# Kernel tuning notes

Hardware: AMD Instinct MI355X
Metric: run time of the kernel (lower is better)

## Reference

```python
import jax, jax.numpy as jnp
import numpy as np

N = 100000   # nodes
E = 1600000  # edges
G = 512      # graphs
IN_F = 128
HID = 64
EPS = 1e-5


def setup_inputs() -> dict:
    key = jax.random.key(0)
    ks = jax.random.split(key, 16)
    x = jax.random.normal(ks[0], (N, IN_F), dtype=jnp.float32)
    edge_index = jax.random.randint(ks[1], (2, E), 0, N, dtype=jnp.int64)
    batch = jnp.sort(jax.random.randint(ks[2], (N,), 0, G, dtype=jnp.int64))
    s = 0.05
    return {
        'x': x, 'edge_index': edge_index, 'batch': batch,
        'W1': jax.random.normal(ks[3], (IN_F, HID), jnp.float32) * s,
        'b1': jax.random.normal(ks[4], (HID,), jnp.float32) * s,
        'g1': jax.random.uniform(ks[5], (HID,), jnp.float32),
        'be1': jax.random.normal(ks[6], (HID,), jnp.float32) * s,
        'rm1': jnp.zeros((HID,), jnp.float32),
        'rv1': jnp.ones((HID,), jnp.float32),
        'W2': jax.random.normal(ks[7], (HID, HID), jnp.float32) * s,
        'b2': jax.random.normal(ks[8], (HID,), jnp.float32) * s,
        'g2': jax.random.uniform(ks[9], (HID,), jnp.float32),
        'be2': jax.random.normal(ks[10], (HID,), jnp.float32) * s,
        'rm2': jnp.zeros((HID,), jnp.float32),
        'rv2': jnp.ones((HID,), jnp.float32),
        'Wh1': jax.random.normal(ks[11], (2 * HID, HID), jnp.float32) * s,
        'bh1': jax.random.normal(ks[12], (HID,), jnp.float32) * s,
        'Wh2': jax.random.normal(ks[13], (HID, HID // 2), jnp.float32) * s,
        'bh2': jnp.zeros((HID // 2,), jnp.float32),
        'Wh3': jax.random.normal(ks[14], (HID // 2, 1), jnp.float32) * s,
        'bh3': jnp.zeros((1,), jnp.float32),
    }


def _gcn(h, W, b, src, dst):
    # GCNConv with added self-loops and symmetric D^{-1/2} A D^{-1/2} normalization
    hw = h @ W                                   # [N, HID]
    deg = jnp.ones((N,), hw.dtype).at[dst].add(1.0)  # in-degree + self-loop
    dinv = jax.lax.rsqrt(deg)
    norm = dinv[src] * dinv[dst]                 # [E]
    agg = jax.ops.segment_sum(hw[src] * norm[:, None], dst, num_segments=N)
    return agg + hw * (dinv * dinv)[:, None] + b  # self-loop term + bias


def _bn(x, g, b, rm, rv):
    return (x - rm) * jax.lax.rsqrt(rv + EPS) * g + b


def reference(x, edge_index, batch, W1, b1, g1, be1, rm1, rv1,
              W2, b2, g2, be2, rm2, rv2, Wh1, bh1, Wh2, bh2, Wh3, bh3):
    src, dst = edge_index[0], edge_index[1]
    # layer 0 (no residual: dim change 128 -> 64)
    h = jax.nn.relu(_bn(_gcn(x, W1, b1, src, dst), g1, be1, rm1, rv1))
    # layer 1 with residual
    h = h + jax.nn.relu(_bn(_gcn(h, W2, b2, src, dst), g2, be2, rm2, rv2))
    # global mean + max pooling per graph
    ones = jnp.ones((N,), h.dtype)
    cnt = jnp.maximum(jax.ops.segment_sum(ones, batch, num_segments=G), 1.0)
    h_mean = jax.ops.segment_sum(h, batch, num_segments=G) / cnt[:, None]
    h_max = jax.ops.segment_max(h, batch, num_segments=G)
    hg = jnp.concatenate([h_mean, h_max], axis=-1)   # [G, 2*HID]
    # MLP head (dropout disabled in eval)
    z = jax.nn.relu(hg @ Wh1 + bh1)
    z = jax.nn.relu(z @ Wh2 + bh2)
    out = z @ Wh3 + bh3
    return jax.nn.sigmoid(out).squeeze(-1)           # [G]
```

## Files before the change

### kernel.cpp

```cpp
#include <hip/hip_runtime.h>
#include <math.h>

#define NN 100000
#define EE 1600000
#define GG 512
#define INF_ 128
#define HID 64
#define EPS 1e-5f

#define NBUK 391
#define P1_TILES 98
#define P1_PAD 104
#define GB_B 25
#define GEMM1_B 1563

typedef unsigned int uint32;
typedef __attribute__((ext_vector_type(8))) short bf16x8;
typedef __attribute__((ext_vector_type(4))) float f32x4;
typedef __attribute__((ext_vector_type(2))) float f32x2;

static __device__ inline uint32 f2bf(float f) {
    uint32 u = __float_as_uint(f);
    return (u + 0x7FFFu + ((u >> 16) & 1u)) >> 16;
}


template <int K, bool SCALE>
__device__ __forceinline__ void gemm_body(const float* __restrict__ X,
        const float* __restrict__ W, const float* __restrict__ dinv,
        uint32* __restrict__ outb, int nrows, int bx,
        unsigned short* __restrict__ Al, unsigned short* __restrict__ Bl) {
    constexpr int KP = K + 8;
    int tid = threadIdx.x;
    for (int i = tid; i < 64 * (K / 2); i += 256) {
        int n = i & 63, kp = i >> 6;
        uint32 lo = f2bf(W[(size_t)(2 * kp) * 64 + n]);
        uint32 hi = f2bf(W[(size_t)(2 * kp + 1) * 64 + n]);
        *(uint32*)&Bl[n * KP + kp * 2] = lo | (hi << 16);
    }
    int r0 = bx * 64;
    const float* Xb = X + (size_t)r0 * K;
    int limit = (nrows - r0) * K;
    for (int f = tid * 4; f < 64 * K; f += 1024) {
        float4 v = {0.f, 0.f, 0.f, 0.f};
        if (f + 3 < limit) v = *(const float4*)&Xb[f];
        int row = f / K, kpos = f % K;
        ushort4 pk;
        pk.x = (unsigned short)f2bf(v.x);
        pk.y = (unsigned short)f2bf(v.y);
        pk.z = (unsigned short)f2bf(v.z);
        pk.w = (unsigned short)f2bf(v.w);
        *(ushort4*)&Al[row * KP + kpos] = pk;
    }
    __syncthreads();
    int lane = tid & 63, wv = tid >> 6;
    int m = lane & 15, quad = lane >> 4;
    f32x4 acc0 = {0.f, 0.f, 0.f, 0.f}, acc1 = acc0, acc2 = acc0, acc3 = acc0;
    int arow = wv * 16 + m;
#pragma unroll
    for (int k0 = 0; k0 < K; k0 += 32) {
        int koff = k0 + quad * 8;
        bf16x8 a = *(const bf16x8*)&Al[arow * KP + koff];
        bf16x8 b0 = *(const bf16x8*)&Bl[(0 * 16 + m) * KP + koff];
        bf16x8 b1 = *(const bf16x8*)&Bl[(1 * 16 + m) * KP + koff];
        bf16x8 b2 = *(const bf16x8*)&Bl[(2 * 16 + m) * KP + koff];
        bf16x8 b3 = *(const bf16x8*)&Bl[(3 * 16 + m) * KP + koff];
        acc0 = __builtin_amdgcn_mfma_f32_16x16x32_bf16(a, b0, acc0, 0, 0, 0);
        acc1 = __builtin_amdgcn_mfma_f32_16x16x32_bf16(a, b1, acc1, 0, 0, 0);
        acc2 = __builtin_amdgcn_mfma_f32_16x16x32_bf16(a, b2, acc2, 0, 0, 0);
        acc3 = __builtin_amdgcn_mfma_f32_16x16x32_bf16(a, b3, acc3, 0, 0, 0);
    }
    float dv[4];
#pragma unroll
    for (int reg = 0; reg < 4; ++reg) {
        int row = r0 + wv * 16 + quad * 4 + reg;
        if (SCALE) dv[reg] = (row < nrows) ? dinv[row] : 0.f;
        else       dv[reg] = 1.f;
    }
    const float* accs[4] = {(const float*)&acc0, (const float*)&acc1,
                            (const float*)&acc2, (const float*)&acc3};
#pragma unroll
    for (int nt = 0; nt < 4; ++nt) {
#pragma unroll
        for (int reg = 0; reg < 4; ++reg) {
            float val = accs[nt][reg] * dv[reg];
            float v1 = __shfl_down(val, 1);
            float v2 = __shfl_down(val, 2);
            float v3 = __shfl_down(val, 3);
            int row = r0 + wv * 16 + quad * 4 + reg;
            if (((m & 3) == 0) && row < nrows) {
                int u = __builtin_amdgcn_cvt_pk_fp8_f32(val, v1, 0, false);
                u = __builtin_amdgcn_cvt_pk_fp8_f32(v2, v3, u, true);
                outb[(size_t)row * 16 + nt * 4 + (m >> 2)] = (uint32)u;
            }
        }
    }
}

__global__ __launch_bounds__(256) void k_mega(const int* __restrict__ ei,
        int* __restrict__ hblk, const int* __restrict__ bat, int* __restrict__ gb,
        const float* __restrict__ x, const float* __restrict__ W1,
        uint32* __restrict__ hwb,
        const float* b1, const float* g1, const float* be1,
        const float* rm1, const float* rv1,
        const float* b2, const float* g2, const float* be2,
        const float* rm2, const float* rv2, float* sc) {
    __shared__ alignas(16) char smem[64 * (INF_ + 8) * 2 * 2];
    int b = blockIdx.x, t = threadIdx.x;
    if (b < P1_TILES) {
        int* h = (int*)smem;
        for (int i = t; i < NBUK; i += 256) h[i] = 0;
        __syncthreads();
        const int4* dst4 = (const int4*)(ei + EE);
        int base4 = b * 4096;
        for (int j = 0; j < 16; ++j) {
            int i4 = base4 + j * 256 + t;
            if (i4 < EE / 4) {
                int4 d = dst4[i4];
                atomicAdd(&h[d.x >> 8], 1);
                atomicAdd(&h[d.y >> 8], 1);
                atomicAdd(&h[d.z >> 8], 1);
                atomicAdd(&h[d.w >> 8], 1);
            }
        }
        __syncthreads();
        for (int i = t; i < NBUK; i += 256) hblk[i * P1_PAD + b] = h[i];
    } else if (b < P1_TILES + GB_B) {
        int gid = (b - P1_TILES) * 256 + t;
        for (int i = gid; i < NN; i += GB_B * 256) {
            int bi = bat[i];
            if (i == 0) {
                for (int g = 0; g <= bi; ++g) gb[g] = 0;
            } else {
                int bp = bat[i - 1];
                for (int g = bp + 1; g <= bi; ++g) gb[g] = i;
            }
            if (i == NN - 1)
                for (int g = bi + 1; g <= GG; ++g) gb[g] = NN;
        }
    } else if (b < P1_TILES + GB_B + 1) {
        if (t < 64) {
            int l = t;
            float s1 = g1[l] * rsqrtf(rv1[l] + EPS);
            sc[l]       = s1;
            sc[64 + l]  = (b1[l] - rm1[l]) * s1 + be1[l];
            float s2 = g2[l] * rsqrtf(rv2[l] + EPS);
            sc[128 + l] = s2;
            sc[192 + l] = (b2[l] - rm2[l]) * s2 + be2[l];
        } else if (t < 80) {
            hwb[(size_t)NN * 16 + (t - 64)] = 0u;
        }
        for (int i = t; i < NBUK * (P1_PAD - P1_TILES); i += 256) {
            int k = i / (P1_PAD - P1_TILES);
            int bb = P1_TILES + i % (P1_PAD - P1_TILES);
            hblk[k * P1_PAD + bb] = 0;
        }
    } else {
        int bx = b - P1_TILES - GB_B - 1;
        unsigned short* Al = (unsigned short*)smem;
        unsigned short* Bl = (unsigned short*)(smem + 64 * (INF_ + 8) * 2);
        gemm_body<INF_, false>(x, W1, nullptr, hwb, NN, bx, Al, Bl);
    }
}

__global__ __launch_bounds__(512) void k_p1b(const int* __restrict__ ei,
                                             const int* __restrict__ hblk,
                                             uint32* __restrict__ pairs,
                                             int* __restrict__ bbase,
                                             int* __restrict__ offs) {
    __shared__ int h[NBUK];
    __shared__ int wsum[8];
    int b = blockIdx.x, t = threadIdx.x;
    int part = 0, c = 0;
    if (t < NBUK) {
        const int4* row = (const int4*)(hblk + t * P1_PAD);
#pragma unroll
        for (int q = 0; q < P1_PAD / 4; ++q) {
            int4 v = row[q];
            c += v.x + v.y + v.z + v.w;
            part += ((4 * q + 0 < b) ? v.x : 0) + ((4 * q + 1 < b) ? v.y : 0)
                  + ((4 * q + 2 < b) ? v.z : 0) + ((4 * q + 3 < b) ? v.w : 0);
        }
    }
    int lane = t & 63, w = t >> 6;
    int v = c;
    for (int d = 1; d < 64; d <<= 1) { int n = __shfl_up(v, d); if (lane >= d) v += n; }
    if (lane == 63) wsum[w] = v;
    __syncthreads();
    int pre = 0;
    for (int q = 0; q < w; ++q) pre += wsum[q];
    int excl = pre + v - c;
    if (t < NBUK) h[t] = excl + part;
    if (b == 0) {
        if (t <= NBUK) bbase[t] = excl;
        if (t == 0) offs[NN] = EE;
    }
    __syncthreads();
    const int4* src4 = (const int4*)ei;
    const int4* dst4 = (const int4*)(ei + EE);
    int base4 = b * 4096;
    for (int j = 0; j < 8; ++j) {
        int i4 = base4 + j * 512 + t;
        if (i4 < EE / 4) {
            int4 d = dst4[i4];
            int4 s = src4[i4];
            int p0 = atomicAdd(&h[d.x >> 8], 1);
            pairs[p0] = ((uint32)s.x << 8) | (uint32)(d.x & 255);
            int p1 = atomicAdd(&h[d.y >> 8], 1);
            pairs[p1] = ((uint32)s.y << 8) | (uint32)(d.y & 255);
            int p2 = atomicAdd(&h[d.z >> 8], 1);
            pairs[p2] = ((uint32)s.z << 8) | (uint32)(d.z & 255);
            int p3 = atomicAdd(&h[d.w >> 8], 1);
            pairs[p3] = ((uint32)s.w << 8) | (uint32)(d.w & 255);
        }
    }
}

__global__ __launch_bounds__(256) void k_p2(const uint32* __restrict__ pairs,
                                            const int* __restrict__ bbase,
                                            int* __restrict__ offs, float* __restrict__ dinv,
                                            int* __restrict__ col) {
    int b = blockIdx.x, t = threadIdx.x;
    int nbase = b << 8;
    int ebase = bbase[b], eend = bbase[b + 1];
    int m = eend - ebase;
    __shared__ int cnt[256];
    __shared__ int wsum[4];
    cnt[t] = 0;
    __syncthreads();
    for (int i = t; i < m; i += 256)
        atomicAdd(&cnt[pairs[ebase + i] & 255u], 1);
    __syncthreads();
    int c = cnt[t];
    int lane = t & 63, w = t >> 6;
    int v = c;
    for (int d = 1; d < 64; d <<= 1) { int n = __shfl_up(v, d); if (lane >= d) v += n; }
    if (lane == 63) wsum[w] = v;
    __syncthreads();
    int pre = 0;
    for (int q = 0; q < w; ++q) pre += wsum[q];
    int excl = pre + v - c;
    int node = nbase + t;
    if (node < NN) {
        offs[node] = ebase + excl;
        dinv[node] = rsqrtf(1.f + (float)c);
    }
    __syncthreads();
    cnt[t] = excl;
    __syncthreads();
    for (int i = t; i < m; i += 256) {
        uint32 u = pairs[ebase + i];
        int loc = atomicAdd(&cnt[u & 255u], 1);
        col[ebase + loc] = (int)(u >> 8);
    }
}

__global__ void k_gcn_gather_w(const uint32* __restrict__ hwb, const int* __restrict__ col,
                               const int* __restrict__ offs,
                               const float* __restrict__ dinv, const float* __restrict__ scale,
                               const float* __restrict__ shift,
                               float* __restrict__ out) {
    int node = blockIdx.x * 4 + (threadIdx.x >> 6);
    if (node >= NN) return;
    int lane = threadIdx.x & 63;
    int quarter = lane >> 4;
    int fl = lane & 15;
    int e0 = offs[node], e1 = offs[node + 1];
    float di = dinv[node];
    uint32 uself = hwb[(size_t)node * 16 + fl];
    float a0 = 0.f, a1 = 0.f, a2 = 0.f, a3 = 0.f;
    float b0 = 0.f, b1 = 0.f, b2 = 0.f, b3 = 0.f;
    for (int base = e0; base < e1; base += 64) {
        int m = e1 - base; if (m > 64) m = 64;
        int srcv = NN; float wv = 0.f;
        if (lane < m) { srcv = col[base + lane]; wv = dinv[srcv]; }
        for (int j = 0; j < m; j += 16) {
            int   s0 = __shfl(srcv, j + quarter);
            int   s1 = __shfl(srcv, j + 4 + quarter);
            int   s2 = __shfl(srcv, j + 8 + quarter);
            int   s3 = __shfl(srcv, j + 12 + quarter);
            float w0 = __shfl(wv, j + quarter);
            float w1 = __shfl(wv, j + 4 + quarter);
            float w2 = __shfl(wv, j + 8 + quarter);
            float w3 = __shfl(wv, j + 12 + quarter);
            uint32 u0 = hwb[(size_t)s0 * 16 + fl];
            uint32 u1 = hwb[(size_t)s1 * 16 + fl];
            uint32 u2 = hwb[(size_t)s2 * 16 + fl];
            uint32 u3 = hwb[(size_t)s3 * 16 + fl];
            f32x2 l0 = __builtin_amdgcn_cvt_pk_f32_fp8((int)u0, false);
            f32x2 h0 = __builtin_amdgcn_cvt_pk_f32_fp8((int)u0, true);
            f32x2 l1 = __builtin_amdgcn_cvt_pk_f32_fp8((int)u1, false);
            f32x2 h1 = __builtin_amdgcn_cvt_pk_f32_fp8((int)u1, true);
            f32x2 l2 = __builtin_amdgcn_cvt_pk_f32_fp8((int)u2, false);
            f32x2 h2 = __builtin_amdgcn_cvt_pk_f32_fp8((int)u2, true);
            f32x2 l3 = __builtin_amdgcn_cvt_pk_f32_fp8((int)u3, false);
            f32x2 h3 = __builtin_amdgcn_cvt_pk_f32_fp8((int)u3, true);
            a0 = fmaf(l0[0], w0, a0); a1 = fmaf(l0[1], w0, a1);
            a2 = fmaf(h0[0], w0, a2); a3 = fmaf(h0[1], w0, a3);
            b0 = fmaf(l1[0], w1, b0); b1 = fmaf(l1[1], w1, b1);
            b2 = fmaf(h1[0], w1, b2); b3 = fmaf(h1[1], w1, b3);
            a0 = fmaf(l2[0], w2, a0); a1 = fmaf(l2[1], w2, a1);
            a2 = fmaf(h2[0], w2, a2); a3 = fmaf(h2[1], w2, a3);
            b0 = fmaf(l3[0], w3, b0); b1 = fmaf(l3[1], w3, b1);
            b2 = fmaf(h3[0], w3, b2); b3 = fmaf(h3[1], w3, b3);
        }
    }
    a0 += b0; a1 += b1; a2 += b2; a3 += b3;
    a0 += __shfl_xor(a0, 16); a0 += __shfl_xor(a0, 32);
    a1 += __shfl_xor(a1, 16); a1 += __shfl_xor(a1, 32);
    a2 += __shfl_xor(a2, 16); a2 += __shfl_xor(a2, 32);
    a3 += __shfl_xor(a3, 16); a3 += __shfl_xor(a3, 32);
    if (quarter == 0) {
        f32x2 slo = __builtin_amdgcn_cvt_pk_f32_fp8((int)uself, false);
        f32x2 shi = __builtin_amdgcn_cvt_pk_f32_fp8((int)uself, true);
        float dii = di * di;
        float4 sc4 = *(const float4*)&scale[4 * fl];
        float4 sh4 = *(const float4*)&shift[4 * fl];
        float v0 = fmaf(a0 * di + slo[0] * dii, sc4.x, sh4.x);
        float v1 = fmaf(a1 * di + slo[1] * dii, sc4.y, sh4.y);
        float v2 = fmaf(a2 * di + shi[0] * dii, sc4.z, sh4.z);
        float v3 = fmaf(a3 * di + shi[1] * dii, sc4.w, sh4.w);
        float4 o;
        o.x = fmaxf(v0, 0.f); o.y = fmaxf(v1, 0.f);
        o.z = fmaxf(v2, 0.f); o.w = fmaxf(v3, 0.f);
        *(float4*)&out[(size_t)node * 64 + 4 * fl] = o;
    }
}

__global__ void k_gcn_gather(const uint32* __restrict__ hwb, const int* __restrict__ col,
                             const int* __restrict__ offs,
                             const float* __restrict__ dinv, const float* __restrict__ scale,
                             const float* __restrict__ shift, const float* __restrict__ resid,
                             float* __restrict__ out) {
    int node = blockIdx.x * 4 + (threadIdx.x >> 6);
    if (node >= NN) return;
    int lane = threadIdx.x & 63;
    int quarter = lane >> 4;
    int fl = lane & 15;
    int e0 = offs[node], e1 = offs[node + 1];
    float di = dinv[node];
    uint32 uself = hwb[(size_t)node * 16 + fl];
    float a0 = 0.f, a1 = 0.f, a2 = 0.f, a3 = 0.f;
    float b0 = 0.f, b1 = 0.f, b2 = 0.f, b3 = 0.f;
    for (int base = e0; base < e1; base += 64) {
        int m = e1 - base; if (m > 64) m = 64;
        int srcv = NN;
        if (lane < m) srcv = col[base + lane];
        for (int j = 0; j < m; j += 16) {
            int s0 = __shfl(srcv, j + quarter);
            int s1 = __shfl(srcv, j + 4 + quarter);
            int s2 = __shfl(srcv, j + 8 + quarter);
            int s3 = __shfl(srcv, j + 12 + quarter);
            uint32 u0 = hwb[(size_t)s0 * 16 + fl];
            uint32 u1 = hwb[(size_t)s1 * 16 + fl];
            uint32 u2 = hwb[(size_t)s2 * 16 + fl];
            uint32 u3 = hwb[(size_t)s3 * 16 + fl];
            f32x2 l0 = __builtin_amdgcn_cvt_pk_f32_fp8((int)u0, false);
            f32x2 h0 = __builtin_amdgcn_cvt_pk_f32_fp8((int)u0, true);
            f32x2 l1 = __builtin_amdgcn_cvt_pk_f32_fp8((int)u1, false);
            f32x2 h1 = __builtin_amdgcn_cvt_pk_f32_fp8((int)u1, true);
            f32x2 l2 = __builtin_amdgcn_cvt_pk_f32_fp8((int)u2, false);
            f32x2 h2 = __builtin_amdgcn_cvt_pk_f32_fp8((int)u2, true);
            f32x2 l3 = __builtin_amdgcn_cvt_pk_f32_fp8((int)u3, false);
            f32x2 h3 = __builtin_amdgcn_cvt_pk_f32_fp8((int)u3, true);
            a0 += l0[0]; a1 += l0[1]; a2 += h0[0]; a3 += h0[1];
            b0 += l1[0]; b1 += l1[1]; b2 += h1[0]; b3 += h1[1];
            a0 += l2[0]; a1 += l2[1]; a2 += h2[0]; a3 += h2[1];
            b0 += l3[0]; b1 += l3[1]; b2 += h3[0]; b3 += h3[1];
        }
    }
    a0 += b0; a1 += b1; a2 += b2; a3 += b3;
    a0 += __shfl_xor(a0, 16); a0 += __shfl_xor(a0, 32);
    a1 += __shfl_xor(a1, 16); a1 += __shfl_xor(a1, 32);
    a2 += __shfl_xor(a2, 16); a2 += __shfl_xor(a2, 32);
    a3 += __shfl_xor(a3, 16); a3 += __shfl_xor(a3, 32);
    if (quarter == 0) {
        f32x2 slo = __builtin_amdgcn_cvt_pk_f32_fp8((int)uself, false);
        f32x2 shi = __builtin_amdgcn_cvt_pk_f32_fp8((int)uself, true);
        float4 sc4 = *(const float4*)&scale[4 * fl];
        float4 sh4 = *(const float4*)&shift[4 * fl];
        float v0 = fmaf((a0 + slo[0]) * di, sc4.x, sh4.x);
        float v1 = fmaf((a1 + slo[1]) * di, sc4.y, sh4.y);
        float v2 = fmaf((a2 + shi[0]) * di, sc4.z, sh4.z);
        float v3 = fmaf((a3 + shi[1]) * di, sc4.w, sh4.w);
        float4 rv = *(const float4*)&resid[(size_t)node * 64 + 4 * fl];
        float4 o;
        o.x = fmaxf(v0, 0.f) + rv.x;
        o.y = fmaxf(v1, 0.f) + rv.y;
        o.z = fmaxf(v2, 0.f) + rv.z;
        o.w = fmaxf(v3, 0.f) + rv.w;
        *(float4*)&out[(size_t)node * 64 + 4 * fl] = o;
    }
}

__global__ void k_poolhead(const float* __restrict__ h, const int* __restrict__ gb,
                           const float* __restrict__ Wh1, const float* __restrict__ bh1,
                           const float* __restrict__ Wh2, const float* __restrict__ bh2,
                           const float* __restrict__ Wh3, const float* __restrict__ bh3,
                           float* __restrict__ out) {
    int g = blockIdx.x, t = threadIdx.x;
    int lo = gb[g], hi = gb[g + 1];
    float s0 = 0.f, s1 = 0.f, s2 = 0.f, s3 = 0.f;
    float s4 = 0.f, s5 = 0.f, s6 = 0.f, s7 = 0.f;
    float m0 = 0.f, m1 = 0.f, m2 = 0.f, m3 = 0.f;
    float m4 = 0.f, m5 = 0.f, m6 = 0.f, m7 = 0.f;
    int i = lo;
    for (; i + 8 <= hi; i += 8) {
        float v0 = h[(size_t)(i + 0) * 64 + t];
        float v1 = h[(size_t)(i + 1) * 64 + t];
        float v2 = h[(size_t)(i + 2) * 64 + t];
        float v3 = h[(size_t)(i + 3) * 64 + t];
        float v4 = h[(size_t)(i + 4) * 64 + t];
        float v5 = h[(size_t)(i + 5) * 64 + t];
        float v6 = h[(size_t)(i + 6) * 64 + t];
        float v7 = h[(size_t)(i + 7) * 64 + t];
        s0 += v0; m0 = fmaxf(m0, v0);
        s1 += v1; m1 = fmaxf(m1, v1);
        s2 += v2; m2 = fmaxf(m2, v2);
        s3 += v3; m3 = fmaxf(m3, v3);
        s4 += v4; m4 = fmaxf(m4, v4);
        s5 += v5; m5 = fmaxf(m5, v5);
        s6 += v6; m6 = fmaxf(m6, v6);
        s7 += v7; m7 = fmaxf(m7, v7);
    }
    for (; i < hi; ++i) {
        float v = h[(size_t)i * 64 + t];
        s0 += v; m0 = fmaxf(m0, v);
    }
    float sum = ((s0 + s1) + (s2 + s3)) + ((s4 + s5) + (s6 + s7));
    float mx = fmaxf(fmaxf(fmaxf(m0, m1), fmaxf(m2, m3)),
                     fmaxf(fmaxf(m4, m5), fmaxf(m6, m7)));
    float c = fmaxf((float)(hi - lo), 1.f);
    __shared__ float hg[128];
    __shared__ float z1[64];
    __shared__ float z2[32];
    hg[t]      = sum / c;
    hg[64 + t] = mx;
    __syncthreads();
    float acc = bh1[t];
#pragma unroll 8
    for (int k = 0; k < 128; ++k) acc = fmaf(hg[k], Wh1[k * 64 + t], acc);
    z1[t] = fmaxf(acc, 0.f);
    __syncthreads();
    if (t < 32) {
        float a2 = bh2[t];
#pragma unroll 8
        for (int k = 0; k < 64; ++k) a2 = fmaf(z1[k], Wh2[k * 32 + t], a2);
        z2[t] = fmaxf(a2, 0.f);
    }
    __syncthreads();
    if (t == 0) {
        float a3 = bh3[0];
        for (int k = 0; k < 32; ++k) a3 = fmaf(z2[k], Wh3[k], a3);
        out[g] = 1.f / (1.f + expf(-a3));
    }
}

__global__ __launch_bounds__(256) void k_gemm2(const float* __restrict__ X,
                                               const float* __restrict__ W,
                                               const float* __restrict__ dinv,
                                               uint32* __restrict__ outb) {
    __shared__ alignas(16) unsigned short Al[64 * (HID + 8)];
    __shared__ alignas(16) unsigned short Bl[64 * (HID + 8)];
    gemm_body<HID, true>(X, W, dinv, outb, NN, blockIdx.x, Al, Bl);
}


static inline size_t alignup(size_t x) { return (x + 255) & ~(size_t)255; }

extern "C" void kernel_launch(void* const* d_in, const int* in_sizes, int n_in,
                              void* d_out, int out_size, void* d_ws, size_t ws_size,
                              hipStream_t stream) {
    const float* x   = (const float*)d_in[0];
    const int*   ei  = (const int*)d_in[1];
    const int*   bat = (const int*)d_in[2];
    const float* W1  = (const float*)d_in[3];
    const float* b1  = (const float*)d_in[4];
    const float* g1  = (const float*)d_in[5];
    const float* be1 = (const float*)d_in[6];
    const float* rm1 = (const float*)d_in[7];
    const float* rv1 = (const float*)d_in[8];
    const float* W2  = (const float*)d_in[9];
    const float* b2  = (const float*)d_in[10];
    const float* g2  = (const float*)d_in[11];
    const float* be2 = (const float*)d_in[12];
    const float* rm2 = (const float*)d_in[13];
    const float* rv2 = (const float*)d_in[14];
    const float* Wh1 = (const float*)d_in[15];
    const float* bh1 = (const float*)d_in[16];
    const float* Wh2 = (const float*)d_in[17];
    const float* bh2 = (const float*)d_in[18];
    const float* Wh3 = (const float*)d_in[19];
    const float* bh3 = (const float*)d_in[20];
    float* out = (float*)d_out;

    char* ws = (char*)d_ws;
    size_t o = 0;
    int*   hblk   = (int*)(ws + o);  o = alignup(o + (size_t)NBUK * P1_PAD * 4);
    int*   bbase  = (int*)(ws + o);  o = alignup(o + (NBUK + 1) * 4);
    int*   offs   = (int*)(ws + o);  o = alignup(o + (NN + 1) * 4);
    uint32* pairs = (uint32*)(ws + o); o = alignup(o + (size_t)EE * 4);
    int*   col    = (int*)(ws + o);  o = alignup(o + (size_t)EE * 4);
    float* dinv   = (float*)(ws + o); o = alignup(o + (size_t)NN * 4);
    float* scb    = (float*)(ws + o); o = alignup(o + 4 * 64 * 4);
    int*   gb     = (int*)(ws + o);  o = alignup(o + (GG + 1) * 4);
    uint32* hwb   = (uint32*)(ws + o); o = alignup(o + (size_t)(NN + 1) * 16 * 4);
    float* h      = (float*)(ws + o); o = alignup(o + (size_t)NN * 64 * 4);
    (void)ws_size; (void)n_in; (void)in_sizes; (void)out_size;

    k_mega<<<P1_TILES + GB_B + 1 + GEMM1_B, 256, 0, stream>>>(
        ei, hblk, bat, gb, x, W1, hwb,
        b1, g1, be1, rm1, rv1, b2, g2, be2, rm2, rv2, scb);
    k_p1b<<<P1_TILES, 512, 0, stream>>>(ei, hblk, pairs, bbase, offs);
    k_p2<<<NBUK, 256, 0, stream>>>(pairs, bbase, offs, dinv, col);

    k_gcn_gather_w<<<(NN + 3) / 4, 256, 0, stream>>>(hwb, col, offs, dinv,
                                                     scb, scb + 64, h);
    k_gemm2<<<GEMM1_B, 256, 0, stream>>>(h, W2, dinv, hwb);
    k_gcn_gather<<<(NN + 3) / 4, 256, 0, stream>>>(hwb, col, offs, dinv,
                                                   scb + 128, scb + 192, h, h);
    k_poolhead<<<GG, 64, 0, stream>>>(h, gb, Wh1, bh1, Wh2, bh2, Wh3, bh3, out);
}
```

Before: 284.8 us.

## Replace per-node gathers with bucket-level LDS-accumulating gather and bf16 h1

Replaces the per-node wave gather (which needed CSR offsets) with a kernel that processes each 256-node bucket in one block. Edges are split evenly across 16 slots, partial sums are accumulated into a shared-memory tile with atomics, and the BN/ReLU epilogue is applied afterwards. The first layer output is stored as bf16, which halves the bytes read by the second GEMM and the residual add. It also removes the offsets array. The cost is far fewer blocks, heavy LDS usage, and long serial per-thread edge loops with limited memory-level parallelism.

```diff
diff --git a/kernel.cpp b/kernel.cpp
--- a/kernel.cpp
+++ b/kernel.cpp
@@ -23,6 +23,8 @@
     uint32 u = __float_as_uint(f);
     return (u + 0x7FFFu + ((u >> 16) & 1u)) >> 16;
 }
+static __device__ inline float bf_lo(uint32 u) { return __uint_as_float(u << 16); }
+static __device__ inline float bf_hi(uint32 u) { return __uint_as_float(u & 0xFFFF0000u); }
 
 
 template <int K, bool SCALE>
@@ -166,8 +168,7 @@
 __global__ __launch_bounds__(512) void k_p1b(const int* __restrict__ ei,
                                              const int* __restrict__ hblk,
                                              uint32* __restrict__ pairs,
-                                             int* __restrict__ bbase,
-                                             int* __restrict__ offs) {
+                                             int* __restrict__ bbase) {
     __shared__ int h[NBUK];
     __shared__ int wsum[8];
     int b = blockIdx.x, t = threadIdx.x;
@@ -191,10 +192,7 @@
     for (int q = 0; q < w; ++q) pre += wsum[q];
     int excl = pre + v - c;
     if (t < NBUK) h[t] = excl + part;
-    if (b == 0) {
-        if (t <= NBUK) bbase[t] = excl;
-        if (t == 0) offs[NN] = EE;
-    }
+    if (b == 0 && t <= NBUK) bbase[t] = excl;
     __syncthreads();
     const int4* src4 = (const int4*)ei;
     const int4* dst4 = (const int4*)(ei + EE);
@@ -218,8 +216,8 @@
 
 __global__ __launch_bounds__(256) void k_p2(const uint32* __restrict__ pairs,
                                             const int* __restrict__ bbase,
-                                            int* __restrict__ offs, float* __restrict__ dinv,
-                                            int* __restrict__ col) {
+                                            float* __restrict__ dinv,
+                                            uint32* __restrict__ col) {
     int b = blockIdx.x, t = threadIdx.x;
     int nbase = b << 8;
     int ebase = bbase[b], eend = bbase[b + 1];
@@ -241,155 +239,112 @@
     for (int q = 0; q < w; ++q) pre += wsum[q];
     int excl = pre + v - c;
     int node = nbase + t;
-    if (node < NN) {
-        offs[node] = ebase + excl;
-        dinv[node] = rsqrtf(1.f + (float)c);
-    }
+    if (node < NN) dinv[node] = rsqrtf(1.f + (float)c);
     __syncthreads();
     cnt[t] = excl;
     __syncthreads();
     for (int i = t; i < m; i += 256) {
         uint32 u = pairs[ebase + i];
         int loc = atomicAdd(&cnt[u & 255u], 1);
-        col[ebase + loc] = (int)(u >> 8);
-    }
-}
-
-__global__ void k_gcn_gather_w(const uint32* __restrict__ hwb, const int* __restrict__ col,
-                               const int* __restrict__ offs,
-                               const float* __restrict__ dinv, const float* __restrict__ scale,
-                               const float* __restrict__ shift,
-                               float* __restrict__ out) {
-    int node = blockIdx.x * 4 + (threadIdx.x >> 6);
-    if (node >= NN) return;
-    int lane = threadIdx.x & 63;
-    int quarter = lane >> 4;
-    int fl = lane & 15;
-    int e0 = offs[node], e1 = offs[node + 1];
-    float di = dinv[node];
-    uint32 uself = hwb[(size_t)node * 16 + fl];
+        col[ebase + loc] = u;
+    }
+}
+
+template <bool WEIGHTED>
+__global__ __launch_bounds__(256) void k_gather_ep(
+        const uint32* __restrict__ hwb, const uint32* __restrict__ colp,
+        const int* __restrict__ bbase, const float* __restrict__ dinv,
+        const float* __restrict__ scale, const float* __restrict__ shift,
+        const uint32* __restrict__ resid, uint32* __restrict__ outb16,
+        float* __restrict__ outf32) {
+    __shared__ float acc[256 * 64];
+    int t = threadIdx.x, b = blockIdx.x;
+    float4 z4 = {0.f, 0.f, 0.f, 0.f};
+    for (int i = t * 4; i < 256 * 64; i += 1024) *(float4*)&acc[i] = z4;
+    __syncthreads();
+    int e0 = bbase[b], e1 = bbase[b + 1];
+    int m = e1 - e0;
+    int lane = t & 63, quarter = lane >> 4, fl = lane & 15, wv = t >> 6;
+    int slot = wv * 4 + quarter;
+    int len = (m + 15) >> 4;
+    int sbeg = e0 + slot * len;
+    int send = sbeg + len; if (send > e1) send = e1;
+    int cur = -1;
     float a0 = 0.f, a1 = 0.f, a2 = 0.f, a3 = 0.f;
-    float b0 = 0.f, b1 = 0.f, b2 = 0.f, b3 = 0.f;
-    for (int base = e0; base < e1; base += 64) {
-        int m = e1 - base; if (m > 64) m = 64;
-        int srcv = NN; float wv = 0.f;
-        if (lane < m) { srcv = col[base + lane]; wv = dinv[srcv]; }
-        for (int j = 0; j < m; j += 16) {
-            int   s0 = __shfl(srcv, j + quarter);
-            int   s1 = __shfl(srcv, j + 4 + quarter);
-            int   s2 = __shfl(srcv, j + 8 + quarter);
-            int   s3 = __shfl(srcv, j + 12 + quarter);
-            float w0 = __shfl(wv, j + quarter);
-            float w1 = __shfl(wv, j + 4 + quarter);
-            float w2 = __shfl(wv, j + 8 + quarter);
-            float w3 = __shfl(wv, j + 12 + quarter);
-            uint32 u0 = hwb[(size_t)s0 * 16 + fl];
-            uint32 u1 = hwb[(size_t)s1 * 16 + fl];
-            uint32 u2 = hwb[(size_t)s2 * 16 + fl];
-            uint32 u3 = hwb[(size_t)s3 * 16 + fl];
-            f32x2 l0 = __builtin_amdgcn_cvt_pk_f32_fp8((int)u0, false);
-            f32x2 h0 = __builtin_amdgcn_cvt_pk_f32_fp8((int)u0, true);
-            f32x2 l1 = __builtin_amdgcn_cvt_pk_f32_fp8((int)u1, false);
-            f32x2 h1 = __builtin_amdgcn_cvt_pk_f32_fp8((int)u1, true);
-            f32x2 l2 = __builtin_amdgcn_cvt_pk_f32_fp8((int)u2, false);
-            f32x2 h2 = __builtin_amdgcn_cvt_pk_f32_fp8((int)u2, true);
-            f32x2 l3 = __builtin_amdgcn_cvt_pk_f32_fp8((int)u3, false);
-            f32x2 h3 = __builtin_amdgcn_cvt_pk_f32_fp8((int)u3, true);
-            a0 = fmaf(l0[0], w0, a0); a1 = fmaf(l0[1], w0, a1);
-            a2 = fmaf(h0[0], w0, a2); a3 = fmaf(h0[1], w0, a3);
-            b0 = fmaf(l1[0], w1, b0); b1 = fmaf(l1[1], w1, b1);
-            b2 = fmaf(h1[0], w1, b2); b3 = fmaf(h1[1], w1, b3);
-            a0 = fmaf(l2[0], w2, a0); a1 = fmaf(l2[1], w2, a1);
-            a2 = fmaf(h2[0], w2, a2); a3 = fmaf(h2[1], w2, a3);
-            b0 = fmaf(l3[0], w3, b0); b1 = fmaf(l3[1], w3, b1);
-            b2 = fmaf(h3[0], w3, b2); b3 = fmaf(h3[1], w3, b3);
-        }
-    }
-    a0 += b0; a1 += b1; a2 += b2; a3 += b3;
-    a0 += __shfl_xor(a0, 16); a0 += __shfl_xor(a0, 32);
-    a1 += __shfl_xor(a1, 16); a1 += __shfl_xor(a1, 32);
-    a2 += __shfl_xor(a2, 16); a2 += __shfl_xor(a2, 32);
-    a3 += __shfl_xor(a3, 16); a3 += __shfl_xor(a3, 32);
-    if (quarter == 0) {
-        f32x2 slo = __builtin_amdgcn_cvt_pk_f32_fp8((int)uself, false);
-        f32x2 shi = __builtin_amdgcn_cvt_pk_f32_fp8((int)uself, true);
-        float dii = di * di;
-        float4 sc4 = *(const float4*)&scale[4 * fl];
-        float4 sh4 = *(const float4*)&shift[4 * fl];
-        float v0 = fmaf(a0 * di + slo[0] * dii, sc4.x, sh4.x);
-        float v1 = fmaf(a1 * di + slo[1] * dii, sc4.y, sh4.y);
-        float v2 = fmaf(a2 * di + shi[0] * dii, sc4.z, sh4.z);
-        float v3 = fmaf(a3 * di + shi[1] * dii, sc4.w, sh4.w);
-        float4 o;
-        o.x = fmaxf(v0, 0.f); o.y = fmaxf(v1, 0.f);
-        o.z = fmaxf(v2, 0.f); o.w = fmaxf(v3, 0.f);
-        *(float4*)&out[(size_t)node * 64 + 4 * fl] = o;
-    }
-}
-
-__global__ void k_gcn_gather(const uint32* __restrict__ hwb, const int* __restrict__ col,
-                             const int* __restrict__ offs,
-                             const float* __restrict__ dinv, const float* __restrict__ scale,
-                             const float* __restrict__ shift, const float* __restrict__ resid,
-                             float* __restrict__ out) {
-    int node = blockIdx.x * 4 + (threadIdx.x >> 6);
-    if (node >= NN) return;
-    int lane = threadIdx.x & 63;
-    int quarter = lane >> 4;
-    int fl = lane & 15;
-    int e0 = offs[node], e1 = offs[node + 1];
-    float di = dinv[node];
-    uint32 uself = hwb[(size_t)node * 16 + fl];
-    float a0 = 0.f, a1 = 0.f, a2 = 0.f, a3 = 0.f;
-    float b0 = 0.f, b1 = 0.f, b2 = 0.f, b3 = 0.f;
-    for (int base = e0; base < e1; base += 64) {
-        int m = e1 - base; if (m > 64) m = 64;
-        int srcv = NN;
-        if (lane < m) srcv = col[base + lane];
-        for (int j = 0; j < m; j += 16) {
-            int s0 = __shfl(srcv, j + quarter);
-            int s1 = __shfl(srcv, j + 4 + quarter);
-            int s2 = __shfl(srcv, j + 8 + quarter);
-            int s3 = __shfl(srcv, j + 12 + quarter);
-            uint32 u0 = hwb[(size_t)s0 * 16 + fl];
-            uint32 u1 = hwb[(size_t)s1 * 16 + fl];
-            uint32 u2 = hwb[(size_t)s2 * 16 + fl];
-            uint32 u3 = hwb[(size_t)s3 * 16 + fl];
-            f32x2 l0 = __builtin_amdgcn_cvt_pk_f32_fp8((int)u0, false);
-            f32x2 h0 = __builtin_amdgcn_cvt_pk_f32_fp8((int)u0, true);
-            f32x2 l1 = __builtin_amdgcn_cvt_pk_f32_fp8((int)u1, false);
-            f32x2 h1 = __builtin_amdgcn_cvt_pk_f32_fp8((int)u1, true);
-            f32x2 l2 = __builtin_amdgcn_cvt_pk_f32_fp8((int)u2, false);
-            f32x2 h2 = __builtin_amdgcn_cvt_pk_f32_fp8((int)u2, true);
-            f32x2 l3 = __builtin_amdgcn_cvt_pk_f32_fp8((int)u3, false);
-            f32x2 h3 = __builtin_amdgcn_cvt_pk_f32_fp8((int)u3, true);
-            a0 += l0[0]; a1 += l0[1]; a2 += h0[0]; a3 += h0[1];
-            b0 += l1[0]; b1 += l1[1]; b2 += h1[0]; b3 += h1[1];
-            a0 += l2[0]; a1 += l2[1]; a2 += h2[0]; a3 += h2[1];
-            b0 += l3[0]; b1 += l3[1]; b2 += h3[0]; b3 += h3[1];
-        }
-    }
-    a0 += b0; a1 += b1; a2 += b2; a3 += b3;
-    a0 += __shfl_xor(a0, 16); a0 += __shfl_xor(a0, 32);
-    a1 += __shfl_xor(a1, 16); a1 += __shfl_xor(a1, 32);
-    a2 += __shfl_xor(a2, 16); a2 += __shfl_xor(a2, 32);
-    a3 += __shfl_xor(a3, 16); a3 += __shfl_xor(a3, 32);
-    if (quarter == 0) {
+    if (sbeg < send) {
+        uint32 u = colp[sbeg];
+        uint32 row = hwb[(size_t)(u >> 8) * 16 + fl];
+        float w = WEIGHTED ? dinv[u >> 8] : 0.f;
+        for (int e = sbeg; e < send; ++e) {
+            int e2 = (e + 1 < send) ? (e + 1) : e;
+            uint32 un = colp[e2];
+            uint32 rown = hwb[(size_t)(un >> 8) * 16 + fl];
+            float wn = WEIGHTED ? dinv[un >> 8] : 0.f;
+            int nl = (int)(u & 255u);
+            if (nl != cur) {
+                if (cur >= 0) {
+                    atomicAdd(&acc[cur * 64 + 4 * fl + 0], a0);
+                    atomicAdd(&acc[cur * 64 + 4 * fl + 1], a1);
+                    atomicAdd(&acc[cur * 64 + 4 * fl + 2], a2);
+                    atomicAdd(&acc[cur * 64 + 4 * fl + 3], a3);
+                }
+                cur = nl; a0 = a1 = a2 = a3 = 0.f;
+            }
+            f32x2 lo = __builtin_amdgcn_cvt_pk_f32_fp8((int)row, false);
+            f32x2 hi = __builtin_amdgcn_cvt_pk_f32_fp8((int)row, true);
+            if (WEIGHTED) {
+                a0 = fmaf(lo[0], w, a0); a1 = fmaf(lo[1], w, a1);
+                a2 = fmaf(hi[0], w, a2); a3 = fmaf(hi[1], w, a3);
+            } else {
+                a0 += lo[0]; a1 += lo[1]; a2 += hi[0]; a3 += hi[1];
+            }
+            u = un; row = rown; w = wn;
+        }
+        if (cur >= 0) {
+            atomicAdd(&acc[cur * 64 + 4 * fl + 0], a0);
+            atomicAdd(&acc[cur * 64 + 4 * fl + 1], a1);
+            atomicAdd(&acc[cur * 64 + 4 * fl + 2], a2);
+            atomicAdd(&acc[cur * 64 + 4 * fl + 3], a3);
+        }
+    }
+    __syncthreads();
+    int nbase = b << 8;
+    for (int r = 0; r < 16; ++r) {
+        int nl = r * 16 + wv * 4 + quarter;
+        int node = nbase + nl;
+        if (node >= NN) continue;
+        float4 s4 = *(float4*)&acc[nl * 64 + 4 * fl];
+        float di = dinv[node];
+        uint32 uself = hwb[(size_t)node * 16 + fl];
         f32x2 slo = __builtin_amdgcn_cvt_pk_f32_fp8((int)uself, false);
         f32x2 shi = __builtin_amdgcn_cvt_pk_f32_fp8((int)uself, true);
         float4 sc4 = *(const float4*)&scale[4 * fl];
         float4 sh4 = *(const float4*)&shift[4 * fl];
-        float v0 = fmaf((a0 + slo[0]) * di, sc4.x, sh4.x);
-        float v1 = fmaf((a1 + slo[1]) * di, sc4.y, sh4.y);
-        float v2 = fmaf((a2 + shi[0]) * di, sc4.z, sh4.z);
-        float v3 = fmaf((a3 + shi[1]) * di, sc4.w, sh4.w);
-        float4 rv = *(const float4*)&resid[(size_t)node * 64 + 4 * fl];
-        float4 o;
-        o.x = fmaxf(v0, 0.f) + rv.x;
-        o.y = fmaxf(v1, 0.f) + rv.y;
-        o.z = fmaxf(v2, 0.f) + rv.z;
-        o.w = fmaxf(v3, 0.f) + rv.w;
-        *(float4*)&out[(size_t)node * 64 + 4 * fl] = o;
+        if (WEIGHTED) {
+            float dii = di * di;
+            float v0 = fmaf(s4.x * di + slo[0] * dii, sc4.x, sh4.x);
+            float v1 = fmaf(s4.y * di + slo[1] * dii, sc4.y, sh4.y);
+            float v2 = fmaf(s4.z * di + shi[0] * dii, sc4.z, sh4.z);
+            float v3 = fmaf(s4.w * di + shi[1] * dii, sc4.w, sh4.w);
+            v0 = fmaxf(v0, 0.f); v1 = fmaxf(v1, 0.f);
+            v2 = fmaxf(v2, 0.f); v3 = fmaxf(v3, 0.f);
+            uint2 o;
+            o.x = f2bf(v0) | (f2bf(v1) << 16);
+            o.y = f2bf(v2) | (f2bf(v3) << 16);
+            *(uint2*)&outb16[(size_t)node * 32 + 2 * fl] = o;
+        } else {
+            float v0 = fmaf((s4.x + slo[0]) * di, sc4.x, sh4.x);
+            float v1 = fmaf((s4.y + slo[1]) * di, sc4.y, sh4.y);
+            float v2 = fmaf((s4.z + shi[0]) * di, sc4.z, sh4.z);
+            float v3 = fmaf((s4.w + shi[1]) * di, sc4.w, sh4.w);
+            uint2 rv = *(const uint2*)&resid[(size_t)node * 32 + 2 * fl];
+            float4 o;
+            o.x = fmaxf(v0, 0.f) + bf_lo(rv.x);
+            o.y = fmaxf(v1, 0.f) + bf_hi(rv.x);
+            o.z = fmaxf(v2, 0.f) + bf_lo(rv.y);
+            o.w = fmaxf(v3, 0.f) + bf_hi(rv.y);
+            *(float4*)&outf32[(size_t)node * 64 + 4 * fl] = o;
+        }
     }
 }
 
@@ -456,13 +411,71 @@
     }
 }
 
-__global__ __launch_bounds__(256) void k_gemm2(const float* __restrict__ X,
+__global__ __launch_bounds__(256) void k_gemm2(const uint32* __restrict__ Xb16,
                                                const float* __restrict__ W,
                                                const float* __restrict__ dinv,
                                                uint32* __restrict__ outb) {
-    __shared__ alignas(16) unsigned short Al[64 * (HID + 8)];
-    __shared__ alignas(16) unsigned short Bl[64 * (HID + 8)];
-    gemm_body<HID, true>(X, W, dinv, outb, NN, blockIdx.x, Al, Bl);
+    constexpr int K = HID, KP = K + 8;
+    __shared__ alignas(16) unsigned short Al[64 * KP];
+    __shared__ alignas(16) unsigned short Bl[64 * KP];
+    int tid = threadIdx.x;
+    for (int i = tid; i < 64 * (K / 2); i += 256) {
+        int n = i & 63, kp = i >> 6;
+        uint32 lo = f2bf(W[(size_t)(2 * kp) * 64 + n]);
+        uint32 hi = f2bf(W[(size_t)(2 * kp + 1) * 64 + n]);
+        *(uint32*)&Bl[n * KP + kp * 2] = lo | (hi << 16);
+    }
+    int r0 = blockIdx.x * 64;
+    const uint32* Xr = Xb16 + (size_t)r0 * 32;
+    int limit = (NN - r0) * 32;
+    for (int f = tid * 4; f < 64 * 32; f += 1024) {
+        uint4 v = {0u, 0u, 0u, 0u};
+        if (f + 3 < limit) v = *(const uint4*)&Xr[f];
+        int row = f >> 5, kpos = (f & 31) * 2;
+        *(uint4*)&Al[row * KP + kpos] = v;
+    }
+    __syncthreads();
+    int lane = tid & 63, wv = tid >> 6;
+    int m = lane & 15, quad = lane >> 4;
+    f32x4 acc0 = {0.f, 0.f, 0.f, 0.f}, acc1 = acc0, acc2 = acc0, acc3 = acc0;
+    int arow = wv * 16 + m;
+#pragma unroll
+    for (int k0 = 0; k0 < K; k0 += 32) {
+        int koff = k0 + quad * 8;
+        bf16x8 a = *(const bf16x8*)&Al[arow * KP + koff];
+        bf16x8 b0 = *(const bf16x8*)&Bl[(0 * 16 + m) * KP + koff];
+        bf16x8 b1 = *(const bf16x8*)&Bl[(1 * 16 + m) * KP + koff];
+        bf16x8 b2 = *(const bf16x8*)&Bl[(2 * 16 + m) * KP + koff];
+        bf16x8 b3 = *(const bf16x8*)&Bl[(3 * 16 + m) * KP + koff];
+        acc0 = __builtin_amdgcn_mfma_f32_16x16x32_bf16(a, b0, acc0, 0, 0, 0);
+        acc1 = __builtin_amdgcn_mfma_f32_16x16x32_bf16(a, b1, acc1, 0, 0, 0);
+        acc2 = __builtin_amdgcn_mfma_f32_16x16x32_bf16(a, b2, acc2, 0, 0, 0);
+        acc3 = __builtin_amdgcn_mfma_f32_16x16x32_bf16(a, b3, acc3, 0, 0, 0);
+    }
+    float dv[4];
+#pragma unroll
+    for (int reg = 0; reg < 4; ++reg) {
+        int row = r0 + wv * 16 + quad * 4 + reg;
+        dv[reg] = (row < NN) ? dinv[row] : 0.f;
+    }
+    const float* accs[4] = {(const float*)&acc0, (const float*)&acc1,
+                            (const float*)&acc2, (const float*)&acc3};
+#pragma unroll
+    for (int nt = 0; nt < 4; ++nt) {
+#pragma unroll
+        for (int reg = 0; reg < 4; ++reg) {
+            float val = accs[nt][reg] * dv[reg];
+            float v1 = __shfl_down(val, 1);
+            float v2 = __shfl_down(val, 2);
+            float v3 = __shfl_down(val, 3);
+            int row = r0 + wv * 16 + quad * 4 + reg;
+            if (((m & 3) == 0) && row < NN) {
+                int u = __builtin_amdgcn_cvt_pk_fp8_f32(val, v1, 0, false);
+                u = __builtin_amdgcn_cvt_pk_fp8_f32(v2, v3, u, true);
+                outb[(size_t)row * 16 + nt * 4 + (m >> 2)] = (uint32)u;
+            }
+        }
+    }
 }
 
 
@@ -498,26 +511,26 @@
     size_t o = 0;
     int*   hblk   = (int*)(ws + o);  o = alignup(o + (size_t)NBUK * P1_PAD * 4);
     int*   bbase  = (int*)(ws + o);  o = alignup(o + (NBUK + 1) * 4);
-    int*   offs   = (int*)(ws + o);  o = alignup(o + (NN + 1) * 4);
     uint32* pairs = (uint32*)(ws + o); o = alignup(o + (size_t)EE * 4);
-    int*   col    = (int*)(ws + o);  o = alignup(o + (size_t)EE * 4);
+    uint32* col   = (uint32*)(ws + o); o = alignup(o + (size_t)EE * 4);
     float* dinv   = (float*)(ws + o); o = alignup(o + (size_t)NN * 4);
     float* scb    = (float*)(ws + o); o = alignup(o + 4 * 64 * 4);
     int*   gb     = (int*)(ws + o);  o = alignup(o + (GG + 1) * 4);
     uint32* hwb   = (uint32*)(ws + o); o = alignup(o + (size_t)(NN + 1) * 16 * 4);
+    uint32* h1b   = (uint32*)(ws + o); o = alignup(o + (size_t)NN * 32 * 4);
     float* h      = (float*)(ws + o); o = alignup(o + (size_t)NN * 64 * 4);
     (void)ws_size; (void)n_in; (void)in_sizes; (void)out_size;
 
     k_mega<<<P1_TILES + GB_B + 1 + GEMM1_B, 256, 0, stream>>>(
         ei, hblk, bat, gb, x, W1, hwb,
         b1, g1, be1, rm1, rv1, b2, g2, be2, rm2, rv2, scb);
-    k_p1b<<<P1_TILES, 512, 0, stream>>>(ei, hblk, pairs, bbase, offs);
-    k_p2<<<NBUK, 256, 0, stream>>>(pairs, bbase, offs, dinv, col);
-
-    k_gcn_gather_w<<<(NN + 3) / 4, 256, 0, stream>>>(hwb, col, offs, dinv,
-                                                     scb, scb + 64, h);
-    k_gemm2<<<GEMM1_B, 256, 0, stream>>>(h, W2, dinv, hwb);
-    k_gcn_gather<<<(NN + 3) / 4, 256, 0, stream>>>(hwb, col, offs, dinv,
-                                                   scb + 128, scb + 192, h, h);
+    k_p1b<<<P1_TILES, 512, 0, stream>>>(ei, hblk, pairs, bbase);
+    k_p2<<<NBUK, 256, 0, stream>>>(pairs, bbase, dinv, col);
+
+    k_gather_ep<true><<<NBUK, 256, 0, stream>>>(hwb, col, bbase, dinv,
+                                                scb, scb + 64, nullptr, h1b, nullptr);
+    k_gemm2<<<GEMM1_B, 256, 0, stream>>>(h1b, W2, dinv, hwb);
+    k_gather_ep<false><<<NBUK, 256, 0, stream>>>(hwb, col, bbase, dinv,
+                                                 scb + 128, scb + 192, h1b, nullptr, h);
     k_poolhead<<<GG, 64, 0, stream>>>(h, gb, Wh1, bh1, Wh2, bh2, Wh3, bh3, out);
 }
```

Measured after the change: 517.8 us. +81.8%, slower.
